# Kernel tuning notes

Measured on AMD Instinct MI355X. Metric: run time of the kernel, lower is better.

The kernel has to match this reference:

```python
import jax, jax.numpy as jnp
import numpy as np

B, T, D = 8, 2048, 1024
DQ = DK = 128   # query_dimension == key_dimension (required by Q @ K^T)
DV = 128        # output_dimension


def setup_inputs() -> dict:
    key = jax.random.key(0)
    ks = jax.random.split(key, 7)
    s = 0.02
    return {
        "x_batch": jax.random.normal(ks[0], (B, T, D), dtype=jnp.float32),
        "Wq": jax.random.normal(ks[1], (D, DQ), dtype=jnp.float32) * s,
        "bq": jax.random.normal(ks[2], (DQ,), dtype=jnp.float32) * s,
        "Wk": jax.random.normal(ks[3], (D, DK), dtype=jnp.float32) * s,
        "bk": jax.random.normal(ks[4], (DK,), dtype=jnp.float32) * s,
        "Wv": jax.random.normal(ks[5], (D, DV), dtype=jnp.float32) * s,
        "bv": jax.random.normal(ks[6], (DV,), dtype=jnp.float32) * s,
    }


def reference(x_batch, Wq, bq, Wk, bk, Wv, bv):
    Q = x_batch @ Wq + bq          # [B,T,DQ]
    K = x_batch @ Wk + bk          # [B,T,DK]
    V = x_batch @ Wv + bv          # [B,T,DV]
    # No 1/sqrt(d) scaling in the original module.
    att = jnp.einsum("bqd,bkd->bqk", Q, K)              # [B,T,T]
    t = att.shape[-1]
    # torch.tril(ones, diagonal=-1): strictly-lower triangle (i > j) -> -inf.
    lower = jnp.tril(jnp.ones((t, t), dtype=bool), k=-1)
    att = jnp.where(lower, -jnp.inf, att)
    # Softmax over dim=-2 (the query/row axis), per key column.
    att = jax.nn.softmax(att, axis=-2)
    return att @ V                                       # [B,T,DV]
```

## Files before the change

### kernel.cpp

```cpp
#include <hip/hip_runtime.h>
#include <hip/hip_bf16.h>

#define T_SEQ 2048
#define D_IN  1024
#define DH    128

#define P_ELEMS_PER_B 2162688
#define P_BYTES (8ull * P_ELEMS_PER_B * 2)

typedef __attribute__((ext_vector_type(8))) short bf16x8;
typedef __attribute__((ext_vector_type(4))) float f32x4;

__device__ inline short f2bf(float f) {
    union { float f; unsigned u; } a; a.f = f;
    unsigned u = a.u;
    return (short)((u + 0x7fffu + ((u >> 16) & 1u)) >> 16);
}
__device__ inline float bf2f(short s) {
    union { unsigned u; float f; } a; a.u = ((unsigned)(unsigned short)s) << 16;
    return a.f;
}

#define GLL16(gsrc, ldst)                                                     \
    __builtin_amdgcn_global_load_lds(                                         \
        (const __attribute__((address_space(1))) void*)(gsrc),                \
        (__attribute__((address_space(3))) void*)(ldst), 16, 0, 0)

__global__ __launch_bounds__(256) void k_prep(const float* __restrict__ x,
                                              const float* __restrict__ Wq,
                                              const float* __restrict__ Wk,
                                              const float* __restrict__ Wv,
                                              short* __restrict__ WT,
                                              short* __restrict__ xb) {
    int bid = blockIdx.x;
    int tid = threadIdx.x;
    if (bid < 1536) {
        int idx = bid * 256 + tid;
        int m = idx >> 17;
        int n = (idx >> 10) & (DH - 1);
        int k = idx & (D_IN - 1);
        const float* W = (m == 0) ? Wq : (m == 1) ? Wk : Wv;
        WT[idx] = f2bf(W[k * DH + n]);
    } else {
        int i = (bid - 1536) * 256 + tid;
        const float4* xs = (const float4*)x + (size_t)i * 2;
        float4 a = xs[0], b = xs[1];
        union { short s[8]; uint4 u; } c;
        c.s[0] = f2bf(a.x); c.s[1] = f2bf(a.y); c.s[2] = f2bf(a.z); c.s[3] = f2bf(a.w);
        c.s[4] = f2bf(b.x); c.s[5] = f2bf(b.y); c.s[6] = f2bf(b.z); c.s[7] = f2bf(b.w);
        ((uint4*)xb)[i] = c.u;
    }
}

__global__ __launch_bounds__(256) void k_qkv(const short* __restrict__ xb,
                                             const short* __restrict__ WT,
                                             const float* __restrict__ bq,
                                             const float* __restrict__ bk,
                                             const float* __restrict__ bv,
                                             short* __restrict__ Qb,
                                             short* __restrict__ Kb,
                                             short* __restrict__ VT) {
    __shared__ char As[2][8192];
    __shared__ char Bs[2][16384];
    int g = blockIdx.y;
    int m0 = blockIdx.x * 64;
    int tid = threadIdx.x;
    int wv = tid >> 6, lane = tid & 63;
    int lr = lane & 15, lg = lane >> 4;
    int wm = wv >> 1, wn = wv & 1;

    const char* Ab = (const char*)(xb + (size_t)m0 * D_IN);
    const char* Bb = (const char*)(WT + (size_t)g * DH * D_IN);
    int soff0 = wv * 1024 + lane * 16;

    const f32x4 z4 = {0.f, 0.f, 0.f, 0.f};
    f32x4 acc[2][4];
#pragma unroll
    for (int i = 0; i < 2; i++)
#pragma unroll
        for (int j = 0; j < 4; j++) acc[i][j] = z4;

#define STAGE(cur, kc)                                                        \
    do {                                                                      \
        _Pragma("unroll")                                                     \
        for (int i = 0; i < 2; i++) {                                         \
            int off = soff0 + i * 4096;                                       \
            int row = off >> 7, col = off & 127;                              \
            int cun = col ^ ((row & 7) << 4);                                 \
            GLL16(Ab + (size_t)row * 2048 + (kc) * 2 + cun,                   \
                  &As[cur][wv * 1024 + i * 4096]);                            \
        }                                                                     \
        _Pragma("unroll")                                                     \
        for (int i = 0; i < 4; i++) {                                         \
            int off = soff0 + i * 4096;                                       \
            int row = off >> 7, col = off & 127;                              \
            int cun = col ^ ((row & 7) << 4);                                 \
            GLL16(Bb + (size_t)row * 2048 + (kc) * 2 + cun,                   \
                  &Bs[cur][wv * 1024 + i * 4096]);                            \
        }                                                                     \
    } while (0)

    STAGE(0, 0);
    __syncthreads();

    int asw = (lr & 7) << 4;
    int cur = 0;
    for (int kc = 0; kc < D_IN; kc += 64) {
        if (kc + 64 < D_IN) STAGE(cur ^ 1, kc + 64);
#pragma unroll
        for (int ks2 = 0; ks2 < 2; ks2++) {
            int cb = (ks2 * 64 + lg * 16) ^ asw;
            bf16x8 af[2], bfr[4];
#pragma unroll
            for (int mt = 0; mt < 2; mt++)
                af[mt] = *(const bf16x8*)(&As[cur][(wm * 32 + mt * 16 + lr) * 128 + cb]);
#pragma unroll
            for (int nt = 0; nt < 4; nt++)
                bfr[nt] = *(const bf16x8*)(&Bs[cur][(wn * 64 + nt * 16 + lr) * 128 + cb]);
#pragma unroll
            for (int mt = 0; mt < 2; mt++)
#pragma unroll
                for (int nt = 0; nt < 4; nt++)
                    acc[mt][nt] = __builtin_amdgcn_mfma_f32_16x16x32_bf16(af[mt], bfr[nt], acc[mt][nt], 0, 0, 0);
        }
        __syncthreads();
        cur ^= 1;
    }

    const float* bias_p = (g == 0) ? bq : (g == 1) ? bk : bv;
#pragma unroll
    for (int nt = 0; nt < 4; nt++) {
        int n = wn * 64 + nt * 16 + lr;
        float bias = bias_p[n];
#pragma unroll
        for (int mt = 0; mt < 2; mt++)
#pragma unroll
            for (int r = 0; r < 4; r++) {
                int row = m0 + wm * 32 + mt * 16 + lg * 4 + r;
                short v16 = f2bf(acc[mt][nt][r] + bias);
                if (g == 0)      Qb[(size_t)row * DH + n] = v16;
                else if (g == 1) Kb[(size_t)row * DH + n] = v16;
                else {
                    int b = row >> 11, t = row & (T_SEQ - 1);
                    VT[((size_t)b * DH + n) * T_SEQ + t] = v16;
                }
            }
    }
#undef STAGE
}

__global__ __launch_bounds__(256) void k_score(const short* __restrict__ Qb,
                                               const short* __restrict__ Kb,
                                               short* __restrict__ P,
                                               float* __restrict__ Zc) {
    __shared__ short pbuf[4][16 * 72];
    int jt = blockIdx.x, qt = blockIdx.y, b = blockIdx.z;
    if (jt < qt) return;
    int tid = threadIdx.x;
    int wv = tid >> 6, lane = tid & 63;
    int lr = lane & 15, lg = lane >> 4;
    int qsub = qt * 64 + wv * 16;

    const short* Qp = Qb + ((size_t)b * T_SEQ + qsub + lr) * DH;
    bf16x8 qf[4];
#pragma unroll
    for (int ks = 0; ks < 4; ks++) qf[ks] = *(const bf16x8*)(Qp + ks * 32 + lg * 8);

    const short* Kbase = Kb + (size_t)b * T_SEQ * DH;
    float* Zb = Zc + (size_t)b * T_SEQ;
    short* pw = &pbuf[wv][0];
    const f32x4 z4 = {0.f, 0.f, 0.f, 0.f};

#pragma unroll
    for (int jsub = 0; jsub < 4; jsub++) {
        f32x4 s = z4;
#pragma unroll
        for (int ks = 0; ks < 4; ks++) {
            bf16x8 kfr = *(const bf16x8*)(Kbase +
                (size_t)(jt * 64 + jsub * 16 + lr) * DH + ks * 32 + lg * 8);
            s = __builtin_amdgcn_mfma_f32_16x16x32_bf16(qf[ks], kfr, s, 0, 0, 0);
        }
        int j = jt * 64 + jsub * 16 + lr;
        float csum = 0.f;
#pragma unroll
        for (int r = 0; r < 4; r++) {
            int q = qsub + lg * 4 + r;
            float p = (j >= q) ? __expf(s[r]) : 0.f;
            csum += p;
            pw[(lg * 4 + r) * 72 + jsub * 16 + lr] = f2bf(p);
        }
        csum += __shfl_xor(csum, 16);
        csum += __shfl_xor(csum, 32);
        if (lg == 0) atomicAdd(&Zb[j], csum);
    }
    int rs = 2048 - 64 * qt;
    short* Pb = P + (size_t)b * P_ELEMS_PER_B + (size_t)2048 * qt * (65 - qt);
    uint4 u0 = *(const uint4*)&pw[lr * 72 + lg * 8];
    uint4 u1 = *(const uint4*)&pw[lr * 72 + 32 + lg * 8];
    size_t rbase = (size_t)(wv * 16 + lr) * rs + (size_t)(jt - qt) * 64;
    *(uint4*)&Pb[rbase + lg * 8] = u0;
    *(uint4*)&Pb[rbase + 32 + lg * 8] = u1;
}

__global__ __launch_bounds__(256) void k_vs(const short* __restrict__ VT,
                                            const float* __restrict__ Zc,
                                            short* __restrict__ VS) {
    int i = blockIdx.x * 256 + threadIdx.x;
    int t8 = i & 255;
    int rest = i >> 8;
    int b = rest >> 7;
    size_t e = (size_t)rest * 2048 + t8 * 8;
    const float* Zp = Zc + (size_t)b * T_SEQ + t8 * 8;
    float4 z0 = *(const float4*)Zp;
    float4 z1 = *(const float4*)(Zp + 4);
    union { short s[8]; uint4 u; } in, ot;
    in.u = *(const uint4*)(VT + e);
    ot.s[0] = f2bf(bf2f(in.s[0]) / z0.x);
    ot.s[1] = f2bf(bf2f(in.s[1]) / z0.y);
    ot.s[2] = f2bf(bf2f(in.s[2]) / z0.z);
    ot.s[3] = f2bf(bf2f(in.s[3]) / z0.w);
    ot.s[4] = f2bf(bf2f(in.s[4]) / z1.x);
    ot.s[5] = f2bf(bf2f(in.s[5]) / z1.y);
    ot.s[6] = f2bf(bf2f(in.s[6]) / z1.z);
    ot.s[7] = f2bf(bf2f(in.s[7]) / z1.w);
    *(uint4*)(VS + e) = ot.u;
}

__global__ __launch_bounds__(256) void k_pv(const short* __restrict__ P,
                                            const short* __restrict__ VS,
                                            float* __restrict__ out) {
    __shared__ char As[2][8192];
    __shared__ char Bs[2][16384];
    int qb = blockIdx.x, half = blockIdx.y, b = blockIdx.z;
    int jlo = max(qb * 64, half * 1024);
    int jhi = (half + 1) * 1024;
    if (jlo >= jhi) return;
    int kclo = jlo - qb * 64, kchi = jhi - qb * 64;
    int rs2 = (2048 - 64 * qb) * 2;

    int tid = threadIdx.x;
    int wv = tid >> 6, lane = tid & 63;
    int lr = lane & 15, lg = lane >> 4;
    int wm = wv >> 1, wn = wv & 1;

    const char* Ab = (const char*)(P + (size_t)b * P_ELEMS_PER_B +
                                   (size_t)2048 * qb * (65 - qb));
    const char* Bb = (const char*)(VS + (size_t)b * DH * T_SEQ);
    int soff0 = wv * 1024 + lane * 16;

    const f32x4 z4 = {0.f, 0.f, 0.f, 0.f};
    f32x4 acc[2][4];
#pragma unroll
    for (int i = 0; i < 2; i++)
#pragma unroll
        for (int j = 0; j < 4; j++) acc[i][j] = z4;

#define STAGE(cur, kc)                                                        \
    do {                                                                      \
        _Pragma("unroll")                                                     \
        for (int i = 0; i < 2; i++) {                                         \
            int off = soff0 + i * 4096;                                       \
            int row = off >> 7, col = off & 127;                              \
            int cun = col ^ ((row & 7) << 4);                                 \
            GLL16(Ab + (size_t)row * rs2 + (kc) * 2 + cun,                    \
                  &As[cur][wv * 1024 + i * 4096]);                            \
        }                                                                     \
        _Pragma("unroll")                                                     \
        for (int i = 0; i < 4; i++) {                                         \
            int off = soff0 + i * 4096;                                       \
            int row = off >> 7, col = off & 127;                              \
            int cun = col ^ ((row & 7) << 4);                                 \
            GLL16(Bb + (size_t)row * 4096 + ((kc) + qb * 64) * 2 + cun,       \
                  &Bs[cur][wv * 1024 + i * 4096]);                            \
        }                                                                     \
    } while (0)

    STAGE(0, kclo);
    __syncthreads();

    int asw = (lr & 7) << 4;
    int cur = 0;
    for (int kc = kclo; kc < kchi; kc += 64) {
        if (kc + 64 < kchi) STAGE(cur ^ 1, kc + 64);
#pragma unroll
        for (int ks2 = 0; ks2 < 2; ks2++) {
            int cb = (ks2 * 64 + lg * 16) ^ asw;
            bf16x8 af[2], bfr[4];
#pragma unroll
            for (int mt = 0; mt < 2; mt++)
                af[mt] = *(const bf16x8*)(&As[cur][(wm * 32 + mt * 16 + lr) * 128 + cb]);
#pragma unroll
            for (int nt = 0; nt < 4; nt++)
                bfr[nt] = *(const bf16x8*)(&Bs[cur][(wn * 64 + nt * 16 + lr) * 128 + cb]);
#pragma unroll
            for (int mt = 0; mt < 2; mt++)
#pragma unroll
                for (int nt = 0; nt < 4; nt++)
                    acc[mt][nt] = __builtin_amdgcn_mfma_f32_16x16x32_bf16(af[mt], bfr[nt], acc[mt][nt], 0, 0, 0);
        }
        __syncthreads();
        cur ^= 1;
    }

#pragma unroll
    for (int nt = 0; nt < 4; nt++) {
        int n = wn * 64 + nt * 16 + lr;
#pragma unroll
        for (int mt = 0; mt < 2; mt++)
#pragma unroll
            for (int r = 0; r < 4; r++) {
                int row = qb * 64 + wm * 32 + mt * 16 + lg * 4 + r;
                atomicAdd(&out[((size_t)b * T_SEQ + row) * DH + n], acc[mt][nt][r]);
            }
    }
#undef STAGE
}

extern "C" void kernel_launch(void* const* d_in, const int* in_sizes, int n_in,
                              void* d_out, int out_size, void* d_ws, size_t ws_size,
                              hipStream_t stream) {
    const float* x  = (const float*)d_in[0];
    const float* Wq = (const float*)d_in[1];
    const float* bq = (const float*)d_in[2];
    const float* Wk = (const float*)d_in[3];
    const float* bk = (const float*)d_in[4];
    const float* Wv = (const float*)d_in[5];
    const float* bv = (const float*)d_in[6];
    float* out = (float*)d_out;

    char* ws = (char*)d_ws;
    short* P  = (short*)ws;
    short* xb = (short*)ws;
    char*  p2 = ws + P_BYTES;
    short* WT = (short*)p2;
    short* Qb = (short*)(p2 + 786432);
    short* Kb = (short*)(p2 + 786432 + 4194304);
    short* VT = (short*)(p2 + 786432 + 2 * 4194304);
    short* VS = (short*)(p2 + 786432 + 3 * 4194304);
    float* Zc = (float*)(p2 + 786432 + 4 * 4194304);

    hipMemsetAsync(out, 0, (size_t)out_size * sizeof(float), stream);
    hipMemsetAsync(Zc, 0, 8 * T_SEQ * sizeof(float), stream);
    hipLaunchKernelGGL(k_prep,  dim3(9728),       dim3(256), 0, stream, x, Wq, Wk, Wv, WT, xb);
    hipLaunchKernelGGL(k_qkv,   dim3(256, 3),     dim3(256), 0, stream, xb, WT, bq, bk, bv, Qb, Kb, VT);
    hipLaunchKernelGGL(k_score, dim3(32, 32, 8),  dim3(256), 0, stream, Qb, Kb, P, Zc);
    hipLaunchKernelGGL(k_vs,    dim3(1024),       dim3(256), 0, stream, VT, Zc, VS);
    hipLaunchKernelGGL(k_pv,    dim3(32, 2, 8),   dim3(256), 0, stream, P, VS, out);
}
```

Before: 234.6 us.

## Loop score kernel over 8 key tiles with double-buffered LDS K staging

Each score block now handles one query tile and a chunk of up to eight key tiles. It keeps Q fragments in registers across the chunk and streams K tiles into swizzled, double-buffered LDS through async global-to-LDS loads. This amortises the Q load and block launch cost, and replaces the scattered per-lane global K reads with staged shared-memory reads that overlap the next tile's load. The trade-offs are a 32KB LDS footprint, a barrier per tile, and fewer, longer blocks, which can leave the triangular workload less evenly balanced.

```diff
diff --git a/kernel.cpp b/kernel.cpp
--- a/kernel.cpp
+++ b/kernel.cpp
@@ -153,9 +153,12 @@
                                                const short* __restrict__ Kb,
                                                short* __restrict__ P,
                                                float* __restrict__ Zc) {
+    __shared__ char Ks[2][16384];
     __shared__ short pbuf[4][16 * 72];
-    int jt = blockIdx.x, qt = blockIdx.y, b = blockIdx.z;
-    if (jt < qt) return;
+    int qt = blockIdx.x, jc = blockIdx.y, b = blockIdx.z;
+    if (qt > jc * 8 + 7) return;
+    int jt0 = max(jc * 8, qt), jtend = jc * 8 + 8;
+
     int tid = threadIdx.x;
     int wv = tid >> 6, lane = tid & 63;
     int lr = lane & 15, lg = lane >> 4;
@@ -166,40 +169,59 @@
 #pragma unroll
     for (int ks = 0; ks < 4; ks++) qf[ks] = *(const bf16x8*)(Qp + ks * 32 + lg * 8);
 
-    const short* Kbase = Kb + (size_t)b * T_SEQ * DH;
+    const char* Kbase = (const char*)(Kb + (size_t)b * T_SEQ * DH);
     float* Zb = Zc + (size_t)b * T_SEQ;
     short* pw = &pbuf[wv][0];
-    const f32x4 z4 = {0.f, 0.f, 0.f, 0.f};
-
-#pragma unroll
-    for (int jsub = 0; jsub < 4; jsub++) {
-        f32x4 s = z4;
-#pragma unroll
-        for (int ks = 0; ks < 4; ks++) {
-            bf16x8 kfr = *(const bf16x8*)(Kbase +
-                (size_t)(jt * 64 + jsub * 16 + lr) * DH + ks * 32 + lg * 8);
-            s = __builtin_amdgcn_mfma_f32_16x16x32_bf16(qf[ks], kfr, s, 0, 0, 0);
-        }
-        int j = jt * 64 + jsub * 16 + lr;
-        float csum = 0.f;
-#pragma unroll
-        for (int r = 0; r < 4; r++) {
-            int q = qsub + lg * 4 + r;
-            float p = (j >= q) ? __expf(s[r]) : 0.f;
-            csum += p;
-            pw[(lg * 4 + r) * 72 + jsub * 16 + lr] = f2bf(p);
-        }
-        csum += __shfl_xor(csum, 16);
-        csum += __shfl_xor(csum, 32);
-        if (lg == 0) atomicAdd(&Zb[j], csum);
-    }
     int rs = 2048 - 64 * qt;
     short* Pb = P + (size_t)b * P_ELEMS_PER_B + (size_t)2048 * qt * (65 - qt);
-    uint4 u0 = *(const uint4*)&pw[lr * 72 + lg * 8];
-    uint4 u1 = *(const uint4*)&pw[lr * 72 + 32 + lg * 8];
-    size_t rbase = (size_t)(wv * 16 + lr) * rs + (size_t)(jt - qt) * 64;
-    *(uint4*)&Pb[rbase + lg * 8] = u0;
-    *(uint4*)&Pb[rbase + 32 + lg * 8] = u1;
+    const f32x4 z4 = {0.f, 0.f, 0.f, 0.f};
+
+#define KSTAGE(cur, jt)                                                       \
+    do { _Pragma("unroll")                                                    \
+        for (int i = 0; i < 4; i++) {                                         \
+            int row = i * 16 + wv * 4 + lg;                                   \
+            int col = (lr * 16) ^ ((row & 7) << 4);                           \
+            GLL16(Kbase + (size_t)((jt) * 64 + row) * 256 + col,              \
+                  &Ks[cur][i * 4096 + wv * 1024]);                            \
+        } } while (0)
+
+    KSTAGE(0, jt0);
+    __syncthreads();
+    int cur = 0;
+    int asw = (lr & 7) << 4;
+    for (int jt = jt0; jt < jtend; jt++) {
+        if (jt + 1 < jtend) KSTAGE(cur ^ 1, jt + 1);
+#pragma unroll
+        for (int jsub = 0; jsub < 4; jsub++) {
+            f32x4 s = z4;
+#pragma unroll
+            for (int ks = 0; ks < 4; ks++) {
+                bf16x8 kfr = *(const bf16x8*)&Ks[cur][(jsub * 16 + lr) * 256 +
+                                                      ((ks * 64 + lg * 16) ^ asw)];
+                s = __builtin_amdgcn_mfma_f32_16x16x32_bf16(qf[ks], kfr, s, 0, 0, 0);
+            }
+            int j = jt * 64 + jsub * 16 + lr;
+            float csum = 0.f;
+#pragma unroll
+            for (int r = 0; r < 4; r++) {
+                int q = qsub + lg * 4 + r;
+                float p = (j >= q) ? __expf(s[r]) : 0.f;
+                csum += p;
+                pw[(lg * 4 + r) * 72 + jsub * 16 + lr] = f2bf(p);
+            }
+            csum += __shfl_xor(csum, 16);
+            csum += __shfl_xor(csum, 32);
+            if (lg == 0) atomicAdd(&Zb[j], csum);
+        }
+        uint4 u0 = *(const uint4*)&pw[lr * 72 + lg * 8];
+        uint4 u1 = *(const uint4*)&pw[lr * 72 + 32 + lg * 8];
+        size_t rbase = (size_t)(wv * 16 + lr) * rs + (size_t)(jt - qt) * 64;
+        *(uint4*)&Pb[rbase + lg * 8] = u0;
+        *(uint4*)&Pb[rbase + 32 + lg * 8] = u1;
+        __syncthreads();
+        cur ^= 1;
+    }
+#undef KSTAGE
 }
 
 __global__ __launch_bounds__(256) void k_vs(const short* __restrict__ VT,
@@ -343,7 +365,7 @@
     hipMemsetAsync(Zc, 0, 8 * T_SEQ * sizeof(float), stream);
     hipLaunchKernelGGL(k_prep,  dim3(9728),       dim3(256), 0, stream, x, Wq, Wk, Wv, WT, xb);
     hipLaunchKernelGGL(k_qkv,   dim3(256, 3),     dim3(256), 0, stream, xb, WT, bq, bk, bv, Qb, Kb, VT);
-    hipLaunchKernelGGL(k_score, dim3(32, 32, 8),  dim3(256), 0, stream, Qb, Kb, P, Zc);
+    hipLaunchKernelGGL(k_score, dim3(32, 4, 8),   dim3(256), 0, stream, Qb, Kb, P, Zc);
     hipLaunchKernelGGL(k_vs,    dim3(1024),       dim3(256), 0, stream, VT, Zc, VS);
     hipLaunchKernelGGL(k_pv,    dim3(32, 2, 8),   dim3(256), 0, stream, P, VS, out);
 }
```

Measured after the change: 193.2 us. -17.6%, faster.
